# Kernel optimization log

Measured on AMD Instinct MI355X. Metric: run time of the kernel, lower is better.

Reference implementation:

```python
import jax, jax.numpy as jnp
import numpy as np

N = 8388608          # edge-triangle incidences
S = 2097152          # number of triangles (segments)
LN_EPS = 1e-5        # torch LayerNorm default
RMS_EPS = 1e-6


def _linear_params(key, din, dout):
    k1, k2 = jax.random.split(key)
    lim = 1.0 / np.sqrt(din)
    W = jax.random.uniform(k1, (din, dout), minval=-lim, maxval=lim, dtype=jnp.float32)
    b = jax.random.uniform(k2, (dout,), minval=-lim, maxval=lim, dtype=jnp.float32)
    return W, b


def setup_inputs() -> dict:
    key = jax.random.key(0)
    ks = jax.random.split(key, 9)
    edge_costs = jax.random.normal(ks[0], (N, 1), dtype=jnp.float32)
    edge_ids_all = jax.random.randint(ks[1], (N,), 0, S, dtype=jnp.int32)
    W1, b1 = _linear_params(ks[2], 1, 8)
    W2, b2 = _linear_params(ks[3], 8, 16)
    W3, b3 = _linear_params(ks[4], 16, 16)   # ResBlock 1 linear
    W4, b4 = _linear_params(ks[5], 16, 16)   # ResBlock 2 linear
    W5, b5 = _linear_params(ks[6], 16, 8)
    W6, b6 = _linear_params(ks[7], 8, 1)
    return {
        'edge_costs': edge_costs,
        'W1': W1, 'b1': b1,
        'g1': jnp.ones(8), 'bb1': jnp.zeros(8),      # LayerNorm(8)
        'W2': W2, 'b2': b2,
        'rw1': jnp.ones(16),                          # RMSNorm in ResBlock1
        'W3': W3, 'b3': b3,
        'g2': jnp.ones(16), 'bb2': jnp.zeros(16),    # LayerNorm(16)
        'rw2': jnp.ones(16),                          # RMSNorm in ResBlock2
        'W4': W4, 'b4': b4,
        'W5': W5, 'b5': b5,
        'g3': jnp.ones(8), 'bb3': jnp.zeros(8),      # LayerNorm(8)
        'W6': W6, 'b6': b6,
        'edge_ids_all': edge_ids_all,
        'num_segments': S,
    }


def _layernorm(x, g, b):
    m = jnp.mean(x, axis=-1, keepdims=True)
    v = jnp.mean((x - m) ** 2, axis=-1, keepdims=True)
    return (x - m) / jnp.sqrt(v + LN_EPS) * g + b


def _rmsnorm(x, w):
    rms = jnp.sqrt(jnp.mean(x ** 2, axis=-1, keepdims=True))
    return x / (rms + RMS_EPS) * w


def _gelu(x):
    return jax.nn.gelu(x, approximate=False)  # torch nn.GELU default (erf)


def _mlp(edge_costs, W1, b1, g1, bb1, W2, b2, rw1, W3, b3, g2, bb2, rw2, W4, b4, W5, b5, g3, bb3, W6, b6):
    h = _gelu(_layernorm(edge_costs @ W1 + b1, g1, bb1))   # [N,8]; Dropout(0.1) is identity in eval
    h = _gelu(h @ W2 + b2)                                  # [N,16]
    h = h + jax.nn.relu(_rmsnorm(h, rw1) @ W3 + b3)         # ResBlock
    h = _layernorm(h, g2, bb2)
    h = h + jax.nn.relu(_rmsnorm(h, rw2) @ W4 + b4)         # ResBlock
    h = _layernorm(_gelu(h @ W5 + b5), g3, bb3)             # [N,8]
    return (h @ W6 + b6)[:, 0]                              # logits [N]


def _scatter_softmax(logits, ids, num_segments):
    seg_max = jax.ops.segment_max(logits, ids, num_segments=num_segments)
    e = jnp.exp(logits - seg_max[ids])
    denom = jax.ops.segment_sum(e, ids, num_segments=num_segments)
    return e / denom[ids]


def reference(edge_costs, W1, b1, g1, bb1, W2, b2, rw1, W3, b3, g2, bb2, rw2, W4, b4, W5, b5, g3, bb3, W6, b6, edge_ids_all, num_segments):
    logits = _mlp(edge_costs, W1, b1, g1, bb1, W2, b2, rw1, W3, b3, g2, bb2, rw2, W4, b4, W5, b5, g3, bb3, W6, b6)
    return _scatter_softmax(logits, edge_ids_all, num_segments)
```

## Files before the change

### kernel.cpp

```cpp
#include <hip/hip_runtime.h>
#include <math.h>


#define LN_EPS  1e-5f
#define RMS_EPS 1e-6f

#define TABN    2048
#define TAB_LO  (-8.0f)
#define TAB_DX  (16.0f / TABN)
#define TAB_INV (TABN / 16.0f)

#define NB      512
#define BSH     12
#define SLICE   4096
#define CAP     18432
#define EPT     16
#define BLK_E   (256 * EPT)
#define DUMP    ((unsigned)NB * CAP)

struct MlpW {
    const float *W1, *b1, *g1, *bb1;
    const float *W2, *b2, *rw1, *W3, *b3, *g2, *bb2, *rw2, *W4, *b4;
    const float *W5, *b5, *g3, *bb3, *W6, *b6;
};

__device__ __forceinline__ float gelu_exact(float x) {
    return 0.5f * x * (1.0f + erff(x * 0.70710678118654752f));
}

__device__ __forceinline__ float mlp_logit(float c, const MlpW p) {
    float h8[8];
#pragma unroll
    for (int j = 0; j < 8; ++j) h8[j] = fmaf(c, p.W1[j], p.b1[j]);
    {
        float m = 0.f;
#pragma unroll
        for (int j = 0; j < 8; ++j) m += h8[j];
        m *= 0.125f;
        float v = 0.f;
#pragma unroll
        for (int j = 0; j < 8; ++j) { float d = h8[j] - m; v = fmaf(d, d, v); }
        float is = rsqrtf(fmaf(v, 0.125f, LN_EPS));
#pragma unroll
        for (int j = 0; j < 8; ++j)
            h8[j] = gelu_exact(fmaf((h8[j] - m) * is, p.g1[j], p.bb1[j]));
    }
    float h[16];
#pragma unroll
    for (int j = 0; j < 16; ++j) {
        float acc = p.b2[j];
#pragma unroll
        for (int i = 0; i < 8; ++i) acc = fmaf(h8[i], p.W2[i * 16 + j], acc);
        h[j] = gelu_exact(acc);
    }
    {
        float ms = 0.f;
#pragma unroll
        for (int i = 0; i < 16; ++i) ms = fmaf(h[i], h[i], ms);
        float inv = 1.0f / (sqrtf(ms * 0.0625f) + RMS_EPS);
        float rn[16];
#pragma unroll
        for (int i = 0; i < 16; ++i) rn[i] = h[i] * inv * p.rw1[i];
#pragma unroll
        for (int j = 0; j < 16; ++j) {
            float acc = p.b3[j];
#pragma unroll
            for (int i = 0; i < 16; ++i) acc = fmaf(rn[i], p.W3[i * 16 + j], acc);
            h[j] += fmaxf(acc, 0.f);
        }
    }
    {
        float m = 0.f;
#pragma unroll
        for (int i = 0; i < 16; ++i) m += h[i];
        m *= 0.0625f;
        float v = 0.f;
#pragma unroll
        for (int i = 0; i < 16; ++i) { float d = h[i] - m; v = fmaf(d, d, v); }
        float is = rsqrtf(fmaf(v, 0.0625f, LN_EPS));
#pragma unroll
        for (int i = 0; i < 16; ++i) h[i] = fmaf((h[i] - m) * is, p.g2[i], p.bb2[i]);
    }
    {
        float ms = 0.f;
#pragma unroll
        for (int i = 0; i < 16; ++i) ms = fmaf(h[i], h[i], ms);
        float inv = 1.0f / (sqrtf(ms * 0.0625f) + RMS_EPS);
        float rn[16];
#pragma unroll
        for (int i = 0; i < 16; ++i) rn[i] = h[i] * inv * p.rw2[i];
#pragma unroll
        for (int j = 0; j < 16; ++j) {
            float acc = p.b4[j];
#pragma unroll
            for (int i = 0; i < 16; ++i) acc = fmaf(rn[i], p.W4[i * 16 + j], acc);
            h[j] += fmaxf(acc, 0.f);
        }
    }
    float z[8];
#pragma unroll
    for (int j = 0; j < 8; ++j) {
        float acc = p.b5[j];
#pragma unroll
        for (int i = 0; i < 16; ++i) acc = fmaf(h[i], p.W5[i * 8 + j], acc);
        z[j] = gelu_exact(acc);
    }
    {
        float m = 0.f;
#pragma unroll
        for (int j = 0; j < 8; ++j) m += z[j];
        m *= 0.125f;
        float v = 0.f;
#pragma unroll
        for (int j = 0; j < 8; ++j) { float d = z[j] - m; v = fmaf(d, d, v); }
        float is = rsqrtf(fmaf(v, 0.125f, LN_EPS));
#pragma unroll
        for (int j = 0; j < 8; ++j) z[j] = fmaf((z[j] - m) * is, p.g3[j], p.bb3[j]);
    }
    float logit = p.b6[0];
#pragma unroll
    for (int j = 0; j < 8; ++j) logit = fmaf(z[j], p.W6[j], logit);
    return logit;
}

__global__ __launch_bounds__(256) void k_init(
    MlpW p, float* __restrict__ tabf, unsigned* __restrict__ cursor)
{
    int i = blockIdx.x * 256 + threadIdx.x;
    if (i <= TABN)
        tabf[i] = expf(mlp_logit(TAB_LO + (float)i * TAB_DX, p));
    if (i < NB)
        cursor[i] = (unsigned)i * CAP;
}

__global__ __launch_bounds__(256) void k_bscatter(
    const float* __restrict__ costs, const int* __restrict__ ids,
    unsigned* __restrict__ cursor, unsigned* __restrict__ regions, int n)
{
    __shared__ unsigned cnt[NB];
    __shared__ unsigned loff[NB + 1];
    __shared__ unsigned gbase[NB];
    __shared__ unsigned tup[BLK_E];
    __shared__ unsigned dst[BLK_E];
    __shared__ unsigned wtot[4], wpre[4];

    const int t = threadIdx.x;
    const int lane = t & 63, wv = t >> 6;
    for (int b = t; b < NB; b += 256) cnt[b] = 0u;
    __syncthreads();

    unsigned myt[EPT];
    unsigned myc[EPT];
    const int base = blockIdx.x * BLK_E + t * EPT;
#pragma unroll
    for (int r = 0; r < EPT / 4; ++r) {
        int i = base + r * 4;
        if (i + 3 < n) {
            float4 c4 = *reinterpret_cast<const float4*>(costs + i);
            int4  id4 = *reinterpret_cast<const int4*>(ids + i);
            float cc[4] = {c4.x, c4.y, c4.z, c4.w};
            int   ii[4] = {id4.x, id4.y, id4.z, id4.w};
#pragma unroll
            for (int j = 0; j < 4; ++j) {
                unsigned id = (unsigned)ii[j];
                float u = (cc[j] - TAB_LO) * TAB_INV;
                u = fminf(fmaxf(u, 0.0f), (float)TABN);
                unsigned uf = (unsigned)(u * 512.0f + 0.5f);
                uf = uf > 0xFFFFFu ? 0xFFFFFu : uf;
                unsigned b = id >> BSH;
                unsigned rkb = atomicAdd(&cnt[b], 1u);
                myt[r * 4 + j] = (uf << 12) | (id & (SLICE - 1));
                myc[r * 4 + j] = (b << 16) | rkb;
            }
        } else {
#pragma unroll
            for (int j = 0; j < 4; ++j) {
                int i2 = i + j;
                if (i2 < n) {
                    unsigned id = (unsigned)ids[i2];
                    float u = (costs[i2] - TAB_LO) * TAB_INV;
                    u = fminf(fmaxf(u, 0.0f), (float)TABN);
                    unsigned uf = (unsigned)(u * 512.0f + 0.5f);
                    uf = uf > 0xFFFFFu ? 0xFFFFFu : uf;
                    unsigned b = id >> BSH;
                    unsigned rkb = atomicAdd(&cnt[b], 1u);
                    myt[r * 4 + j] = (uf << 12) | (id & (SLICE - 1));
                    myc[r * 4 + j] = (b << 16) | rkb;
                } else {
                    myc[r * 4 + j] = 0xFFFFFFFFu;
                }
            }
        }
    }
    __syncthreads();

    for (int b = t; b < NB; b += 256)
        gbase[b] = atomicAdd(&cursor[b], cnt[b]);

    {
        unsigned a0 = cnt[2 * t], a1 = cnt[2 * t + 1];
        unsigned s = a0 + a1;
        unsigned v = s;
#pragma unroll
        for (int d = 1; d < 64; d <<= 1) {
            unsigned w = __shfl_up(v, d);
            if (lane >= d) v += w;
        }
        if (lane == 63) wtot[wv] = v;
        __syncthreads();
        if (t == 0) {
            unsigned run = 0;
#pragma unroll
            for (int w = 0; w < 4; ++w) { wpre[w] = run; run += wtot[w]; }
        }
        __syncthreads();
        unsigned incl = v + wpre[wv];
        unsigned excl = incl - s;
        loff[2 * t] = excl;
        loff[2 * t + 1] = excl + a0;
        if (t == 255) loff[NB] = incl;
    }
    __syncthreads();

#pragma unroll
    for (int e = 0; e < EPT; ++e) {
        unsigned c = myc[e];
        if (c != 0xFFFFFFFFu) {
            unsigned b = c >> 16, rkb = c & 0xFFFFu;
            unsigned rk = loff[b] + rkb;
            unsigned d = gbase[b] + rkb;
            tup[rk] = myt[e];
            dst[rk] = (d < (b + 1u) * CAP) ? d : DUMP;
        }
    }
    __syncthreads();

    unsigned stot = loff[NB];
    for (unsigned s = t; s < stot; s += 256)
        regions[dst[s]] = tup[s];
}

__global__ __launch_bounds__(512) void k_reduce(
    const unsigned* __restrict__ regions, const unsigned* __restrict__ cursor,
    const float* __restrict__ tabf, _Float16* __restrict__ rdenom)
{
    __shared__ float slice[SLICE];
    __shared__ float tabl[TABN + 1];
    int b = blockIdx.x, t = threadIdx.x;
    for (int i = t; i <= TABN; i += 512) tabl[i] = tabf[i];
    for (int j = t; j < SLICE; j += 512) slice[j] = 0.f;
    __syncthreads();

    unsigned nb = cursor[b] - (unsigned)b * CAP;
    if (nb > CAP) nb = CAP;
    size_t base = (size_t)b * CAP;
    for (unsigned k = t; k < nb; k += 512) {
        unsigned tp = regions[base + k];
        unsigned idl = tp & (SLICE - 1);
        unsigned uf = tp >> 12;
        unsigned ix = uf >> 9;
        float fr = (float)(uf & 511u) * (1.0f / 512.0f);
        float a = tabl[ix];
        float e = fmaf(fr, tabl[ix + 1] - a, a);
        atomicAdd(&slice[idl], e);
    }
    __syncthreads();
    for (int j = t; j < SLICE; j += 512)
        rdenom[(size_t)b * SLICE + j] = (_Float16)(1.0f / slice[j]);
}

__global__ __launch_bounds__(256) void k_norm(
    const float* __restrict__ costs, const int* __restrict__ ids,
    const float* __restrict__ tabf, const _Float16* __restrict__ rdenom,
    float* __restrict__ out, int n)
{
    __shared__ float tabl[TABN + 1];
    for (int i = threadIdx.x; i <= TABN; i += 256) tabl[i] = tabf[i];
    __syncthreads();

    int stride = gridDim.x * 256 * 4;
    for (int i0 = (blockIdx.x * 256 + threadIdx.x) * 4; i0 < n; i0 += stride) {
        if (i0 + 3 < n) {
            float4 c4 = *reinterpret_cast<const float4*>(costs + i0);
            int4  id4 = *reinterpret_cast<const int4*>(ids + i0);
            float cc[4] = {c4.x, c4.y, c4.z, c4.w};
            int   ii[4] = {id4.x, id4.y, id4.z, id4.w};
            float oo[4];
#pragma unroll
            for (int j = 0; j < 4; ++j) {
                float u = (cc[j] - TAB_LO) * TAB_INV;
                u = fminf(fmaxf(u, 0.0f), (float)TABN - 0.001f);
                int ix = (int)u;
                float fr = u - (float)ix;
                float a = tabl[ix];
                float e = fmaf(fr, tabl[ix + 1] - a, a);
                oo[j] = e * (float)rdenom[ii[j]];
            }
            float4 o; o.x = oo[0]; o.y = oo[1]; o.z = oo[2]; o.w = oo[3];
            *reinterpret_cast<float4*>(out + i0) = o;
        } else {
            for (int i = i0; i < n; ++i) {
                float u = (costs[i] - TAB_LO) * TAB_INV;
                u = fminf(fmaxf(u, 0.0f), (float)TABN - 0.001f);
                int ix = (int)u;
                float fr = u - (float)ix;
                float a = tabl[ix];
                out[i] = fmaf(fr, tabl[ix + 1] - a, a) * (float)rdenom[ids[i]];
            }
        }
    }
}

extern "C" void kernel_launch(void* const* d_in, const int* in_sizes, int n_in,
                              void* d_out, int out_size, void* d_ws, size_t ws_size,
                              hipStream_t stream) {
    const float* costs = (const float*)d_in[0];
    MlpW p;
    p.W1  = (const float*)d_in[1];  p.b1  = (const float*)d_in[2];
    p.g1  = (const float*)d_in[3];  p.bb1 = (const float*)d_in[4];
    p.W2  = (const float*)d_in[5];  p.b2  = (const float*)d_in[6];
    p.rw1 = (const float*)d_in[7];
    p.W3  = (const float*)d_in[8];  p.b3  = (const float*)d_in[9];
    p.g2  = (const float*)d_in[10]; p.bb2 = (const float*)d_in[11];
    p.rw2 = (const float*)d_in[12];
    p.W4  = (const float*)d_in[13]; p.b4  = (const float*)d_in[14];
    p.W5  = (const float*)d_in[15]; p.b5  = (const float*)d_in[16];
    p.g3  = (const float*)d_in[17]; p.bb3 = (const float*)d_in[18];
    p.W6  = (const float*)d_in[19]; p.b6  = (const float*)d_in[20];
    const int* ids = (const int*)d_in[21];

    const int n = in_sizes[0];
    constexpr int S = NB * SLICE;
    const int nblk = (n + BLK_E - 1) / BLK_E;

    unsigned*  regions = (unsigned*)d_ws;
    unsigned*  cursor  = regions + (size_t)NB * CAP + 64;
    float*     tabf    = (float*)(cursor + NB);
    _Float16*  rdenom  = (_Float16*)(tabf + TABN + 1);

    k_init<<<(TABN + 256) / 256, 256, 0, stream>>>(p, tabf, cursor);
    k_bscatter<<<nblk, 256, 0, stream>>>(costs, ids, cursor, regions, n);
    k_reduce<<<NB, 512, 0, stream>>>(regions, cursor, tabf, rdenom);
    k_norm<<<2048, 256, 0, stream>>>(costs, ids, tabf, rdenom, (float*)d_out, n);
}
```

Before: 302.6 us.

## Use nontemporal loads, compact bucket staging, and widen reduce blocks

Streaming loads of costs, ids and region tuples now use nontemporal hints so they pollute the cache less. The scatter kernel stores a 16-bit bucket index per staged element instead of a 32-bit destination, and recomputes the slot from gbase and loff during the write-out, which shrinks shared memory. The reduce kernel moves from 512 to 1024 threads per block to add parallelism per bucket. The extra address arithmetic in the write-out loop, and the higher LDS atomic contention from more threads per block, could offset these savings.

Result: slower. 323.4 us (+6.9%).

```diff
diff --git a/kernel.cpp b/kernel.cpp
--- a/kernel.cpp
+++ b/kernel.cpp
@@ -17,6 +17,9 @@
 #define EPT     16
 #define BLK_E   (256 * EPT)
 #define DUMP    ((unsigned)NB * CAP)
+
+typedef float f32x4 __attribute__((ext_vector_type(4)));
+typedef int   i32x4 __attribute__((ext_vector_type(4)));
 
 struct MlpW {
     const float *W1, *b1, *g1, *bb1;
@@ -141,7 +144,7 @@
     __shared__ unsigned loff[NB + 1];
     __shared__ unsigned gbase[NB];
     __shared__ unsigned tup[BLK_E];
-    __shared__ unsigned dst[BLK_E];
+    __shared__ unsigned short bkt[BLK_E];
     __shared__ unsigned wtot[4], wpre[4];
 
     const int t = threadIdx.x;
@@ -156,14 +159,14 @@
     for (int r = 0; r < EPT / 4; ++r) {
         int i = base + r * 4;
         if (i + 3 < n) {
-            float4 c4 = *reinterpret_cast<const float4*>(costs + i);
-            int4  id4 = *reinterpret_cast<const int4*>(ids + i);
-            float cc[4] = {c4.x, c4.y, c4.z, c4.w};
-            int   ii[4] = {id4.x, id4.y, id4.z, id4.w};
+            f32x4 c4 = __builtin_nontemporal_load(
+                reinterpret_cast<const f32x4*>(costs + i));
+            i32x4 id4 = __builtin_nontemporal_load(
+                reinterpret_cast<const i32x4*>(ids + i));
 #pragma unroll
             for (int j = 0; j < 4; ++j) {
-                unsigned id = (unsigned)ii[j];
-                float u = (cc[j] - TAB_LO) * TAB_INV;
+                unsigned id = (unsigned)id4[j];
+                float u = (c4[j] - TAB_LO) * TAB_INV;
                 u = fminf(fmaxf(u, 0.0f), (float)TABN);
                 unsigned uf = (unsigned)(u * 512.0f + 0.5f);
                 uf = uf > 0xFFFFFu ? 0xFFFFFu : uf;
@@ -228,34 +231,37 @@
         if (c != 0xFFFFFFFFu) {
             unsigned b = c >> 16, rkb = c & 0xFFFFu;
             unsigned rk = loff[b] + rkb;
-            unsigned d = gbase[b] + rkb;
             tup[rk] = myt[e];
-            dst[rk] = (d < (b + 1u) * CAP) ? d : DUMP;
+            bkt[rk] = (unsigned short)b;
         }
     }
     __syncthreads();
 
     unsigned stot = loff[NB];
-    for (unsigned s = t; s < stot; s += 256)
-        regions[dst[s]] = tup[s];
-}
-
-__global__ __launch_bounds__(512) void k_reduce(
+    for (unsigned s = t; s < stot; s += 256) {
+        unsigned b = bkt[s];
+        unsigned slot = gbase[b] + (s - loff[b]);
+        if (slot >= (b + 1u) * CAP) slot = DUMP;
+        regions[slot] = tup[s];
+    }
+}
+
+__global__ __launch_bounds__(1024) void k_reduce(
     const unsigned* __restrict__ regions, const unsigned* __restrict__ cursor,
     const float* __restrict__ tabf, _Float16* __restrict__ rdenom)
 {
     __shared__ float slice[SLICE];
     __shared__ float tabl[TABN + 1];
     int b = blockIdx.x, t = threadIdx.x;
-    for (int i = t; i <= TABN; i += 512) tabl[i] = tabf[i];
-    for (int j = t; j < SLICE; j += 512) slice[j] = 0.f;
+    for (int i = t; i <= TABN; i += 1024) tabl[i] = tabf[i];
+    for (int j = t; j < SLICE; j += 1024) slice[j] = 0.f;
     __syncthreads();
 
     unsigned nb = cursor[b] - (unsigned)b * CAP;
     if (nb > CAP) nb = CAP;
     size_t base = (size_t)b * CAP;
-    for (unsigned k = t; k < nb; k += 512) {
-        unsigned tp = regions[base + k];
+    for (unsigned k = t; k < nb; k += 1024) {
+        unsigned tp = __builtin_nontemporal_load(regions + base + k);
         unsigned idl = tp & (SLICE - 1);
         unsigned uf = tp >> 12;
         unsigned ix = uf >> 9;
@@ -265,7 +271,7 @@
         atomicAdd(&slice[idl], e);
     }
     __syncthreads();
-    for (int j = t; j < SLICE; j += 512)
+    for (int j = t; j < SLICE; j += 1024)
         rdenom[(size_t)b * SLICE + j] = (_Float16)(1.0f / slice[j]);
 }
 
@@ -281,20 +287,20 @@
     int stride = gridDim.x * 256 * 4;
     for (int i0 = (blockIdx.x * 256 + threadIdx.x) * 4; i0 < n; i0 += stride) {
         if (i0 + 3 < n) {
-            float4 c4 = *reinterpret_cast<const float4*>(costs + i0);
-            int4  id4 = *reinterpret_cast<const int4*>(ids + i0);
-            float cc[4] = {c4.x, c4.y, c4.z, c4.w};
-            int   ii[4] = {id4.x, id4.y, id4.z, id4.w};
+            f32x4 c4 = __builtin_nontemporal_load(
+                reinterpret_cast<const f32x4*>(costs + i0));
+            i32x4 id4 = __builtin_nontemporal_load(
+                reinterpret_cast<const i32x4*>(ids + i0));
             float oo[4];
 #pragma unroll
             for (int j = 0; j < 4; ++j) {
-                float u = (cc[j] - TAB_LO) * TAB_INV;
+                float u = (c4[j] - TAB_LO) * TAB_INV;
                 u = fminf(fmaxf(u, 0.0f), (float)TABN - 0.001f);
                 int ix = (int)u;
                 float fr = u - (float)ix;
                 float a = tabl[ix];
                 float e = fmaf(fr, tabl[ix + 1] - a, a);
-                oo[j] = e * (float)rdenom[ii[j]];
+                oo[j] = e * (float)rdenom[id4[j]];
             }
             float4 o; o.x = oo[0]; o.y = oo[1]; o.z = oo[2]; o.w = oo[3];
             *reinterpret_cast<float4*>(out + i0) = o;
@@ -340,6 +346,6 @@
 
     k_init<<<(TABN + 256) / 256, 256, 0, stream>>>(p, tabf, cursor);
     k_bscatter<<<nblk, 256, 0, stream>>>(costs, ids, cursor, regions, n);
-    k_reduce<<<NB, 512, 0, stream>>>(regions, cursor, tabf, rdenom);
+    k_reduce<<<NB, 1024, 0, stream>>>(regions, cursor, tabf, rdenom);
     k_norm<<<2048, 256, 0, stream>>>(costs, ids, tabf, rdenom, (float*)d_out, n);
 }
```
